# Kernel tuning notes

Hardware: AMD Instinct MI355X
Metric: run time of the kernel (lower is better)

## Reference

```python
import jax, jax.numpy as jnp
import numpy as np

H = 4  # num_heads
LN_EPS = 1e-5


def setup_inputs() -> dict:
    key = jax.random.key(0)
    ks = jax.random.split(key, 6)
    B, N, IN, OUT = 4, 2048, 256, 256
    return {
        "node_feats": jax.random.normal(ks[0], (B, N, IN), dtype=jnp.float32),
        "adj_matrix": jax.random.uniform(ks[1], (B, N, N), dtype=jnp.float32),
        "W_lin": jax.random.normal(ks[2], (IN, OUT), dtype=jnp.float32) * (IN ** -0.5),
        "b_lin": jnp.zeros((OUT,), dtype=jnp.float32),
        "W_q": jax.random.normal(ks[3], (IN, OUT), dtype=jnp.float32) * (IN ** -0.5),
        "W_k": jax.random.normal(ks[4], (IN, OUT), dtype=jnp.float32) * (IN ** -0.5),
        "ln_g": jnp.ones((OUT,), dtype=jnp.float32),
        "ln_b": jnp.zeros((OUT,), dtype=jnp.float32),
    }


def _heads(x, B, N):
    # [B,N,OUT] -> [B,H,N,hd]
    return x.reshape(B, N, H, -1).transpose(0, 2, 1, 3)


def reference(node_feats, adj_matrix, W_lin, b_lin, W_q, W_k, ln_g, ln_b):
    B, N, _ = node_feats.shape
    out_dim = W_lin.shape[1]
    hd = out_dim // H
    scale = hd ** -0.5
    lrelu = lambda z: jax.nn.leaky_relu(z, 0.01)

    X = _heads(lrelu(node_feats @ W_lin + b_lin), B, N)   # [B,H,N,hd]
    q = _heads(lrelu(node_feats @ W_q), B, N)
    k = _heads(lrelu(node_feats @ W_k), B, N)

    att = jax.nn.sigmoid(jnp.einsum('bhxd,bhyd->bhxy', q, k) * scale)
    adj_h = adj_matrix[:, None] * att                     # [B,H,N,N]

    # symmetric degree normalization: D^-1/2 A D^-1/2 (broadcast form of diag_embed matmuls)
    deg = jnp.sum(adj_h, axis=-1)                         # [B,H,N]
    dis = jnp.where(deg > 0, deg ** -0.5, 0.0)
    A = dis[..., :, None] * adj_h * dis[..., None, :]

    Y = jnp.einsum('bhxy,bhyd->bhxd', A, X)
    Y = Y.transpose(0, 2, 1, 3).reshape(B, N, out_dim)

    mu = jnp.mean(Y, axis=-1, keepdims=True)
    var = jnp.mean((Y - mu) ** 2, axis=-1, keepdims=True)
    return (Y - mu) * jax.lax.rsqrt(var + LN_EPS) * ln_g + ln_b
```

## Files before the change

kernel.cpp:

```cpp
#include <hip/hip_runtime.h>
#include <hip/hip_bf16.h>

#define B_   4
#define N_   2048
#define IN_  256
#define OUT_ 256
#define H_   4
#define HD_  64
#define LN_EPS 1e-5f

typedef __bf16 bf16x8 __attribute__((ext_vector_type(8)));
typedef float  f32x4  __attribute__((ext_vector_type(4)));
typedef unsigned short u16x8 __attribute__((ext_vector_type(8)));
typedef unsigned int   u32x4 __attribute__((ext_vector_type(4)));

__device__ __forceinline__ unsigned short f2bf(float x) {
    unsigned int u = __float_as_uint(x);
    return (unsigned short)((u + 0x7FFFu + ((u >> 16) & 1u)) >> 16);
}
__device__ __forceinline__ float bf2f(unsigned short u) {
    return __uint_as_float((unsigned int)u << 16);
}
__device__ __forceinline__ unsigned int cvtpk(float lo, float hi) {
    unsigned int r;
    asm("v_cvt_pk_bf16_f32 %0, %1, %2" : "=v"(r) : "v"(lo), "v"(hi));
    return r;
}

__global__ __launch_bounds__(256) void conv_kernel(
    const float* __restrict__ nf, const float* __restrict__ Wl,
    const float* __restrict__ Wq, const float* __restrict__ Wk,
    unsigned short* __restrict__ nfb, unsigned short* __restrict__ Wt)
{
    const int bid = blockIdx.x, tid = threadIdx.x;
    if (bid < 1024) {
        size_t i = ((size_t)bid * 256 + tid) * 8;
        u16x8 o;
        #pragma unroll
        for (int j = 0; j < 8; j++) o[j] = f2bf(nf[i + j]);
        *(u16x8*)&nfb[i] = o;
    } else {
        int t = (bid - 1024) * 256 + tid;
        int z = t >> 16;
        int l = t & 65535;
        int k = l & 255, n = l >> 8;
        const float* W = (z == 0) ? Wl : (z == 1 ? Wq : Wk);
        Wt[(size_t)z * 65536 + n * 256 + k] = f2bf(W[k * 256 + n]);
    }
}

__global__ __launch_bounds__(256) void gemm3_kernel(
    const unsigned short* __restrict__ nfb, const unsigned short* __restrict__ Wt3,
    const float* __restrict__ bl,
    unsigned short* __restrict__ qb, unsigned short* __restrict__ kb,
    unsigned short* __restrict__ Xt)
{
    const int z  = blockIdx.z;
    const int m0 = blockIdx.x * 64, n0 = blockIdx.y * 64;
    const int tid = threadIdx.x, wave = tid >> 6, lane = tid & 63;
    const int lq = lane >> 4, lr = lane & 15;
    const unsigned short* Wt = Wt3 + (size_t)z * 65536;

    f32x4 acc[4] = {};
    #pragma unroll 4
    for (int k0 = 0; k0 < IN_; k0 += 32) {
        bf16x8 af = *(const bf16x8*)&nfb[(size_t)(m0 + wave * 16 + lr) * IN_ + k0 + lq * 8];
        #pragma unroll
        for (int f = 0; f < 4; f++) {
            bf16x8 bfr = *(const bf16x8*)&Wt[(size_t)(n0 + f * 16 + lr) * IN_ + k0 + lq * 8];
            acc[f] = __builtin_amdgcn_mfma_f32_16x16x32_bf16(af, bfr, acc[f], 0, 0, 0);
        }
    }

    #pragma unroll
    for (int f = 0; f < 4; f++) {
        int c = n0 + f * 16 + lr;
        float bias = (z == 0) ? bl[c] : 0.0f;
        #pragma unroll
        for (int r = 0; r < 4; r++) {
            int m = m0 + wave * 16 + lq * 4 + r;
            float v = acc[f][r] + bias;
            v = (v >= 0.f) ? v : 0.01f * v;
            unsigned short bv = f2bf(v);
            if (z == 0) {
                int n = m & (N_ - 1);
                int h = c >> 6, d = c & 63;
                Xt[(((size_t)(m >> 11) * H_ + h) * HD_ + d) * N_ + n] = bv;
            } else {
                unsigned short* dst = (z == 1) ? qb : kb;
                dst[(size_t)m * OUT_ + c] = bv;
            }
        }
    }
}

__global__ __launch_bounds__(256) void att_kernel(
    const float* __restrict__ adj,
    const unsigned short* __restrict__ qb,
    const unsigned short* __restrict__ kb,
    unsigned short* __restrict__ W,
    float* __restrict__ degp,
    int b_base, int SH)
{
    const int s  = blockIdx.z;
    const int bg = b_base + (s >> 2);
    const int hg = s & 3;
    const int x0 = blockIdx.x * 128, y0 = blockIdx.y * 128;
    const int tid = threadIdx.x, wave = tid >> 6, lane = tid & 63;
    const int lq = lane >> 4, lr = lane & 15;
    const int wq = wave >> 1, wn = wave & 1;
    const int wx0 = x0 + wq * 64, wy0 = y0 + wn * 64;
    const float sc = -0.125f * 1.44269504088896f;

    const unsigned short* qrow = qb + (size_t)(bg * N_ + wx0) * OUT_ + hg * HD_;
    const unsigned short* krow = kb + (size_t)(bg * N_ + wy0) * OUT_ + hg * HD_;

    f32x4 acc[4][4] = {};
    #pragma unroll
    for (int ks = 0; ks < 2; ks++) {
        bf16x8 af[4], bf[4];
        #pragma unroll
        for (int mf = 0; mf < 4; mf++)
            af[mf] = *(const bf16x8*)&qrow[(size_t)(mf * 16 + lr) * OUT_ + ks * 32 + lq * 8];
        #pragma unroll
        for (int nf = 0; nf < 4; nf++)
            bf[nf] = *(const bf16x8*)&krow[(size_t)(nf * 16 + lr) * OUT_ + ks * 32 + lq * 8];
        #pragma unroll
        for (int mf = 0; mf < 4; mf++)
            #pragma unroll
            for (int nf = 0; nf < 4; nf++)
                acc[mf][nf] = __builtin_amdgcn_mfma_f32_16x16x32_bf16(af[mf], bf[nf], acc[mf][nf], 0, 0, 0);
    }

    unsigned short* Wp = W + (size_t)s * N_ * N_;
    #pragma unroll
    for (int mf = 0; mf < 4; mf++) {
        #pragma unroll
        for (int r = 0; r < 4; r++) {
            int x = wx0 + mf * 16 + lq * 4 + r;
            const float* arow = adj + ((size_t)bg * N_ + x) * N_ + wy0;
            unsigned short* wrow = Wp + (size_t)x * N_ + wy0;
            float sum = 0.f;
            #pragma unroll
            for (int nf = 0; nf < 4; nf++) {
                float a = arow[nf * 16 + lr];
                float att = __builtin_amdgcn_rcpf(1.f + exp2f(acc[mf][nf][r] * sc));
                float wv = a * att;
                sum += wv;
                wrow[nf * 16 + lr] = f2bf(wv);
            }
            sum += __shfl_xor(sum, 1); sum += __shfl_xor(sum, 2);
            sum += __shfl_xor(sum, 4); sum += __shfl_xor(sum, 8);
            if (lr == 0)
                degp[((size_t)(blockIdx.y * 2 + wn) * SH + s) * N_ + x] = sum;
        }
    }
}

__global__ __launch_bounds__(256) void degsum_kernel(
    const float* __restrict__ degp, float* __restrict__ dis, int b_base, int SH)
{
    int t = blockIdx.x * 256 + threadIdx.x;
    int s = t >> 11, x = t & (N_ - 1);
    float sum = 0.f;
    #pragma unroll
    for (int j = 0; j < 32; j++) sum += degp[((size_t)j * SH + s) * N_ + x];
    dis[((size_t)b_base * H_ + s) * N_ + x] = (sum > 0.f) ? rsqrtf(sum) : 0.f;
}

__global__ __launch_bounds__(256) void scale_kernel(
    const unsigned short* __restrict__ Xt, const float* __restrict__ dis,
    unsigned short* __restrict__ Xs)
{
    int t = blockIdx.x * 256 + threadIdx.x;
    size_t idx = (size_t)t * 8;
    int s = t >> 14;
    int y = (int)(idx & (N_ - 1));
    f32x4 d0 = *(const f32x4*)&dis[(size_t)s * N_ + y];
    f32x4 d1 = *(const f32x4*)&dis[(size_t)s * N_ + y + 4];
    u16x8 x = *(const u16x8*)&Xt[idx];
    u32x4 o;
    o[0] = cvtpk(bf2f(x[0]) * d0[0], bf2f(x[1]) * d0[1]);
    o[1] = cvtpk(bf2f(x[2]) * d0[2], bf2f(x[3]) * d0[3]);
    o[2] = cvtpk(bf2f(x[4]) * d1[0], bf2f(x[5]) * d1[1]);
    o[3] = cvtpk(bf2f(x[6]) * d1[2], bf2f(x[7]) * d1[3]);
    *(u32x4*)&Xs[idx] = o;
}

__global__ __launch_bounds__(512) void yout_kernel(
    const unsigned short* __restrict__ W,
    const unsigned short* __restrict__ Xs,
    const float* __restrict__ dis,
    float* __restrict__ Yraw,
    int b_base)
{
    const int s  = blockIdx.y;
    const int bg = b_base + (s >> 2);
    const int hg = s & 3;
    const int x0 = blockIdx.x * 32;
    const int tid = threadIdx.x;
    const int wave = tid >> 6, lane = tid & 63;
    const int xw = wave >> 2, dq = wave & 3;
    const int lq = lane >> 4, lr = lane & 15;

    __shared__ unsigned short As[2][32 * 256];

    const int srow = tid >> 4, kslot = tid & 15;
    const int swz  = (srow & 7) << 4;
    const unsigned short* Wrow =
        W + (size_t)s * N_ * N_ + (size_t)(x0 + srow) * N_ + kslot * 16;

    const unsigned short* Xp = Xs + ((size_t)s * HD_ + dq * 16 + lr) * N_;

    const int arow = xw * 16 + lr;
    const int arsw = (arow & 7) << 4;

    f32x4 Y = {};

    {
        u16x8 r0 = *(const u16x8*)&Wrow[0];
        u16x8 r1 = *(const u16x8*)&Wrow[8];
        char* base = (char*)&As[0][0] + srow * 512;
        *(u16x8*)(base + ((kslot * 32) ^ swz))      = r0;
        *(u16x8*)(base + ((kslot * 32 + 16) ^ swz)) = r1;
    }
    __syncthreads();

    int cur = 0;
    for (int kt = 0; kt < 8; kt++) {
        u16x8 n0, n1;
        if (kt < 7) {
            n0 = *(const u16x8*)&Wrow[(kt + 1) * 256];
            n1 = *(const u16x8*)&Wrow[(kt + 1) * 256 + 8];
        }
        const char* abase = (const char*)&As[cur][0] + arow * 512;
        #pragma unroll
        for (int half = 0; half < 2; half++) {
            bf16x8 xf[4];
            #pragma unroll
            for (int u = 0; u < 4; u++)
                xf[u] = *(const bf16x8*)&Xp[kt * 256 + (half * 4 + u) * 32 + lq * 8];
            #pragma unroll
            for (int u = 0; u < 4; u++) {
                const int kb = ((half * 4 + u) * 32 + lq * 8) * 2;
                bf16x8 af = *(const bf16x8*)(abase + (kb ^ arsw));
                Y = __builtin_amdgcn_mfma_f32_16x16x32_bf16(af, xf[u], Y, 0, 0, 0);
            }
        }
        if (kt < 7) {
            char* base = (char*)&As[cur ^ 1][0] + srow * 512;
            *(u16x8*)(base + ((kslot * 32) ^ swz))      = n0;
            *(u16x8*)(base + ((kslot * 32 + 16) ^ swz)) = n1;
        }
        __syncthreads();
        cur ^= 1;
    }

    #pragma unroll
    for (int r = 0; r < 4; r++) {
        int x = x0 + xw * 16 + lq * 4 + r;
        float dx = dis[((size_t)bg * H_ + hg) * N_ + x];
        Yraw[((size_t)(bg * N_ + x)) * OUT_ + hg * HD_ + dq * 16 + lr] = Y[r] * dx;
    }
}

__global__ __launch_bounds__(256) void ln_kernel(
    const float* __restrict__ Yraw,
    const float* __restrict__ lng, const float* __restrict__ lnb,
    float* __restrict__ out)
{
    const int row = blockIdx.x;
    const int c = threadIdx.x;
    const size_t base = (size_t)row * OUT_ + c;
    float v = Yraw[base];

    float s1 = v, s2 = v * v;
    #pragma unroll
    for (int d = 1; d < 64; d <<= 1) { s1 += __shfl_xor(s1, d); s2 += __shfl_xor(s2, d); }
    __shared__ float red[2][4];
    if ((c & 63) == 0) { red[0][c >> 6] = s1; red[1][c >> 6] = s2; }
    __syncthreads();
    float t1 = red[0][0] + red[0][1] + red[0][2] + red[0][3];
    float t2 = red[1][0] + red[1][1] + red[1][2] + red[1][3];
    float mu  = t1 * (1.f / 256.f);
    float var = t2 * (1.f / 256.f) - mu * mu;
    float rs  = rsqrtf(var + LN_EPS);
    out[base] = (v - mu) * rs * lng[c] + lnb[c];
}

extern "C" void kernel_launch(void* const* d_in, const int* in_sizes, int n_in,
                              void* d_out, int out_size, void* d_ws, size_t ws_size,
                              hipStream_t stream) {
    const float* nf  = (const float*)d_in[0];
    const float* adj = (const float*)d_in[1];
    const float* Wl  = (const float*)d_in[2];
    const float* bl  = (const float*)d_in[3];
    const float* Wq  = (const float*)d_in[4];
    const float* Wk  = (const float*)d_in[5];
    const float* lng = (const float*)d_in[6];
    const float* lnb = (const float*)d_in[7];
    float* out = (float*)d_out;

    char* w = (char*)d_ws;
    unsigned short* nfb = (unsigned short*)w;  w += (size_t)B_ * N_ * IN_ * 2;
    unsigned short* Wt  = (unsigned short*)w;  w += (size_t)3 * IN_ * OUT_ * 2;
    unsigned short* qb  = (unsigned short*)w;  w += (size_t)B_ * N_ * OUT_ * 2;
    unsigned short* kb  = (unsigned short*)w;  w += (size_t)B_ * N_ * OUT_ * 2;
    unsigned short* Xt  = (unsigned short*)w;  w += (size_t)B_ * N_ * OUT_ * 2;
    unsigned short* Xs  = (unsigned short*)w;  w += (size_t)B_ * N_ * OUT_ * 2;
    float* dis  = (float*)w;                   w += (size_t)B_ * H_ * N_ * 4;
    float* Yraw = (float*)w;                   w += (size_t)B_ * N_ * OUT_ * 4;
    size_t fixed = (size_t)(w - (char*)d_ws);

    size_t need4 = fixed + (size_t)32 * 16 * N_ * 4 + (size_t)16 * N_ * N_ * 2;
    int nb = (ws_size >= need4) ? 4 : 1;
    int SH = nb * H_;
    float* degp = (float*)w;                   w += (size_t)32 * SH * N_ * 4;
    unsigned short* Wbuf = (unsigned short*)w;

    conv_kernel <<<1792, 256, 0, stream>>>(nf, Wl, Wq, Wk, nfb, Wt);
    gemm3_kernel<<<dim3(128, 4, 3), 256, 0, stream>>>(nfb, Wt, bl, qb, kb, Xt);

    for (int b0 = 0; b0 < B_; b0 += nb) {
        size_t xoff = (size_t)b0 * H_ * HD_ * N_;
        att_kernel   <<<dim3(16, 16, SH), 256, 0, stream>>>(adj, qb, kb, Wbuf, degp, b0, SH);
        degsum_kernel<<<SH * N_ / 256, 256, 0, stream>>>(degp, dis, b0, SH);
        scale_kernel <<<SH * HD_ * N_ / 8 / 256, 256, 0, stream>>>(Xt + xoff, dis + (size_t)b0 * H_ * N_, Xs + xoff);
        yout_kernel  <<<dim3(N_ / 32, SH), 512, 0, stream>>>(Wbuf, Xs + xoff, dis, Yraw, b0);
    }
    ln_kernel<<<B_ * N_, 256, 0, stream>>>(Yraw, lng, lnb, out);
}
```

Baseline: 312.8 us.

## Stage adj tile in LDS, coalesce W stores, atomically accumulate degree

The attention kernel now loads the 128x128 adjacency tile into shared memory with coalesced float4 loads. It computes the sigmoid-weighted values in place in LDS and writes the bf16 W tile out as coalesced 16-byte rows, instead of scattered per-lane 2-byte loads and stores. The per-tile partial degree buffer and the degsum kernel are removed: row sums are accumulated with atomicAdd into a zeroed degree array, and rsqrt is taken lazily in the scale and output kernels. This removes one launch and the partial-sum traffic. In exchange it adds atomics, a memset, and rounds adj to bf16 before the multiply, which slightly changes precision.

Result: no change. 313.4 us (+0.2%).

```diff
diff --git a/kernel.cpp b/kernel.cpp
--- a/kernel.cpp
+++ b/kernel.cpp
@@ -12,6 +12,7 @@
 typedef __bf16 bf16x8 __attribute__((ext_vector_type(8)));
 typedef float  f32x4  __attribute__((ext_vector_type(4)));
 typedef unsigned short u16x8 __attribute__((ext_vector_type(8)));
+typedef unsigned int   u32x2 __attribute__((ext_vector_type(2)));
 typedef unsigned int   u32x4 __attribute__((ext_vector_type(4)));
 
 __device__ __forceinline__ unsigned short f2bf(float x) {
@@ -99,7 +100,7 @@
     const unsigned short* __restrict__ qb,
     const unsigned short* __restrict__ kb,
     unsigned short* __restrict__ W,
-    float* __restrict__ degp,
+    float* __restrict__ deg,
     int b_base, int SH)
 {
     const int s  = blockIdx.z;
@@ -109,88 +110,106 @@
     const int tid = threadIdx.x, wave = tid >> 6, lane = tid & 63;
     const int lq = lane >> 4, lr = lane & 15;
     const int wq = wave >> 1, wn = wave & 1;
-    const int wx0 = x0 + wq * 64, wy0 = y0 + wn * 64;
+    const int wx0 = wq * 64, wy0 = wn * 64;
     const float sc = -0.125f * 1.44269504088896f;
 
-    const unsigned short* qrow = qb + (size_t)(bg * N_ + wx0) * OUT_ + hg * HD_;
-    const unsigned short* krow = kb + (size_t)(bg * N_ + wy0) * OUT_ + hg * HD_;
-
+    __shared__ unsigned short ads[128][136];
+
+    {
+        const int row0 = tid >> 5;
+        const int col  = (tid & 31) * 4;
+        const float* ap = adj + ((size_t)bg * N_ + x0 + row0) * N_ + y0 + col;
+        #pragma unroll 4
+        for (int i = 0; i < 16; i++) {
+            f32x4 v = *(const f32x4*)(ap + (size_t)i * 8 * N_);
+            u32x2 p = { cvtpk(v[0], v[1]), cvtpk(v[2], v[3]) };
+            *(u32x2*)&ads[row0 + i * 8][col] = p;
+        }
+    }
+
+    const unsigned short* qrow = qb + (size_t)(bg * N_ + x0 + wx0) * OUT_ + hg * HD_;
+    const unsigned short* krow = kb + (size_t)(bg * N_ + y0 + wy0) * OUT_ + hg * HD_;
     f32x4 acc[4][4] = {};
     #pragma unroll
     for (int ks = 0; ks < 2; ks++) {
-        bf16x8 af[4], bf[4];
+        bf16x8 af[4];
         #pragma unroll
         for (int mf = 0; mf < 4; mf++)
             af[mf] = *(const bf16x8*)&qrow[(size_t)(mf * 16 + lr) * OUT_ + ks * 32 + lq * 8];
         #pragma unroll
-        for (int nf = 0; nf < 4; nf++)
-            bf[nf] = *(const bf16x8*)&krow[(size_t)(nf * 16 + lr) * OUT_ + ks * 32 + lq * 8];
-        #pragma unroll
-        for (int mf = 0; mf < 4; mf++)
+        for (int nf = 0; nf < 4; nf++) {
+            bf16x8 bfr = *(const bf16x8*)&krow[(size_t)(nf * 16 + lr) * OUT_ + ks * 32 + lq * 8];
             #pragma unroll
-            for (int nf = 0; nf < 4; nf++)
-                acc[mf][nf] = __builtin_amdgcn_mfma_f32_16x16x32_bf16(af[mf], bf[nf], acc[mf][nf], 0, 0, 0);
-    }
-
-    unsigned short* Wp = W + (size_t)s * N_ * N_;
+            for (int mf = 0; mf < 4; mf++)
+                acc[mf][nf] = __builtin_amdgcn_mfma_f32_16x16x32_bf16(af[mf], bfr, acc[mf][nf], 0, 0, 0);
+        }
+    }
+    __syncthreads();
+
+    float* degrow = deg + ((size_t)bg * H_ + hg) * N_ + x0;
     #pragma unroll
     for (int mf = 0; mf < 4; mf++) {
         #pragma unroll
         for (int r = 0; r < 4; r++) {
-            int x = wx0 + mf * 16 + lq * 4 + r;
-            const float* arow = adj + ((size_t)bg * N_ + x) * N_ + wy0;
-            unsigned short* wrow = Wp + (size_t)x * N_ + wy0;
+            const int xl = wx0 + mf * 16 + lq * 4 + r;
             float sum = 0.f;
             #pragma unroll
             for (int nf = 0; nf < 4; nf++) {
-                float a = arow[nf * 16 + lr];
+                const int yl = wy0 + nf * 16 + lr;
+                float a = bf2f(ads[xl][yl]);
                 float att = __builtin_amdgcn_rcpf(1.f + exp2f(acc[mf][nf][r] * sc));
                 float wv = a * att;
+                ads[xl][yl] = (unsigned short)cvtpk(wv, wv);
                 sum += wv;
-                wrow[nf * 16 + lr] = f2bf(wv);
             }
             sum += __shfl_xor(sum, 1); sum += __shfl_xor(sum, 2);
             sum += __shfl_xor(sum, 4); sum += __shfl_xor(sum, 8);
             if (lr == 0)
-                degp[((size_t)(blockIdx.y * 2 + wn) * SH + s) * N_ + x] = sum;
-        }
-    }
-}
-
-__global__ __launch_bounds__(256) void degsum_kernel(
-    const float* __restrict__ degp, float* __restrict__ dis, int b_base, int SH)
-{
-    int t = blockIdx.x * 256 + threadIdx.x;
-    int s = t >> 11, x = t & (N_ - 1);
-    float sum = 0.f;
-    #pragma unroll
-    for (int j = 0; j < 32; j++) sum += degp[((size_t)j * SH + s) * N_ + x];
-    dis[((size_t)b_base * H_ + s) * N_ + x] = (sum > 0.f) ? rsqrtf(sum) : 0.f;
+                atomicAdd(&degrow[xl], sum);
+        }
+    }
+    __syncthreads();
+
+    unsigned short* Wp = W + (size_t)s * N_ * N_;
+    const int col = (tid & 15) * 8;
+    const int r0  = tid >> 4;
+    #pragma unroll
+    for (int i = 0; i < 8; i++) {
+        int row = i * 16 + r0;
+        u16x8 v = *(const u16x8*)&ads[row][col];
+        *(u16x8*)&Wp[(size_t)(x0 + row) * N_ + y0 + col] = v;
+    }
 }
 
 __global__ __launch_bounds__(256) void scale_kernel(
-    const unsigned short* __restrict__ Xt, const float* __restrict__ dis,
+    const unsigned short* __restrict__ Xt, const float* __restrict__ deg,
     unsigned short* __restrict__ Xs)
 {
     int t = blockIdx.x * 256 + threadIdx.x;
     size_t idx = (size_t)t * 8;
     int s = t >> 14;
     int y = (int)(idx & (N_ - 1));
-    f32x4 d0 = *(const f32x4*)&dis[(size_t)s * N_ + y];
-    f32x4 d1 = *(const f32x4*)&dis[(size_t)s * N_ + y + 4];
+    f32x4 g0 = *(const f32x4*)&deg[(size_t)s * N_ + y];
+    f32x4 g1 = *(const f32x4*)&deg[(size_t)s * N_ + y + 4];
+    float dv[8];
+    #pragma unroll
+    for (int j = 0; j < 4; j++) {
+        dv[j]     = (g0[j] > 0.f) ? rsqrtf(g0[j]) : 0.f;
+        dv[4 + j] = (g1[j] > 0.f) ? rsqrtf(g1[j]) : 0.f;
+    }
     u16x8 x = *(const u16x8*)&Xt[idx];
     u32x4 o;
-    o[0] = cvtpk(bf2f(x[0]) * d0[0], bf2f(x[1]) * d0[1]);
-    o[1] = cvtpk(bf2f(x[2]) * d0[2], bf2f(x[3]) * d0[3]);
-    o[2] = cvtpk(bf2f(x[4]) * d1[0], bf2f(x[5]) * d1[1]);
-    o[3] = cvtpk(bf2f(x[6]) * d1[2], bf2f(x[7]) * d1[3]);
+    o[0] = cvtpk(bf2f(x[0]) * dv[0], bf2f(x[1]) * dv[1]);
+    o[1] = cvtpk(bf2f(x[2]) * dv[2], bf2f(x[3]) * dv[3]);
+    o[2] = cvtpk(bf2f(x[4]) * dv[4], bf2f(x[5]) * dv[5]);
+    o[3] = cvtpk(bf2f(x[6]) * dv[6], bf2f(x[7]) * dv[7]);
     *(u32x4*)&Xs[idx] = o;
 }
 
 __global__ __launch_bounds__(512) void yout_kernel(
     const unsigned short* __restrict__ W,
     const unsigned short* __restrict__ Xs,
-    const float* __restrict__ dis,
+    const float* __restrict__ deg,
     float* __restrict__ Yraw,
     int b_base)
 {
@@ -259,7 +278,8 @@
     #pragma unroll
     for (int r = 0; r < 4; r++) {
         int x = x0 + xw * 16 + lq * 4 + r;
-        float dx = dis[((size_t)bg * H_ + hg) * N_ + x];
+        float g = deg[((size_t)bg * H_ + hg) * N_ + x];
+        float dx = (g > 0.f) ? rsqrtf(g) : 0.f;
         Yraw[((size_t)(bg * N_ + x)) * OUT_ + hg * HD_ + dq * 16 + lr] = Y[r] * dx;
     }
 }
@@ -308,25 +328,24 @@
     unsigned short* kb  = (unsigned short*)w;  w += (size_t)B_ * N_ * OUT_ * 2;
     unsigned short* Xt  = (unsigned short*)w;  w += (size_t)B_ * N_ * OUT_ * 2;
     unsigned short* Xs  = (unsigned short*)w;  w += (size_t)B_ * N_ * OUT_ * 2;
-    float* dis  = (float*)w;                   w += (size_t)B_ * H_ * N_ * 4;
+    float* deg  = (float*)w;                   w += (size_t)B_ * H_ * N_ * 4;
     float* Yraw = (float*)w;                   w += (size_t)B_ * N_ * OUT_ * 4;
     size_t fixed = (size_t)(w - (char*)d_ws);
 
-    size_t need4 = fixed + (size_t)32 * 16 * N_ * 4 + (size_t)16 * N_ * N_ * 2;
+    size_t need4 = fixed + (size_t)16 * N_ * N_ * 2;
     int nb = (ws_size >= need4) ? 4 : 1;
     int SH = nb * H_;
-    float* degp = (float*)w;                   w += (size_t)32 * SH * N_ * 4;
     unsigned short* Wbuf = (unsigned short*)w;
 
+    hipMemsetAsync(deg, 0, (size_t)B_ * H_ * N_ * 4, stream);
     conv_kernel <<<1792, 256, 0, stream>>>(nf, Wl, Wq, Wk, nfb, Wt);
     gemm3_kernel<<<dim3(128, 4, 3), 256, 0, stream>>>(nfb, Wt, bl, qb, kb, Xt);
 
     for (int b0 = 0; b0 < B_; b0 += nb) {
         size_t xoff = (size_t)b0 * H_ * HD_ * N_;
-        att_kernel   <<<dim3(16, 16, SH), 256, 0, stream>>>(adj, qb, kb, Wbuf, degp, b0, SH);
-        degsum_kernel<<<SH * N_ / 256, 256, 0, stream>>>(degp, dis, b0, SH);
-        scale_kernel <<<SH * HD_ * N_ / 8 / 256, 256, 0, stream>>>(Xt + xoff, dis + (size_t)b0 * H_ * N_, Xs + xoff);
-        yout_kernel  <<<dim3(N_ / 32, SH), 512, 0, stream>>>(Wbuf, Xs + xoff, dis, Yraw, b0);
+        att_kernel  <<<dim3(16, 16, SH), 256, 0, stream>>>(adj, qb, kb, Wbuf, deg, b0, SH);
+        scale_kernel<<<SH * HD_ * N_ / 8 / 256, 256, 0, stream>>>(Xt + xoff, deg + (size_t)b0 * H_ * N_, Xs + xoff);
+        yout_kernel <<<dim3(N_ / 32, SH), 512, 0, stream>>>(Wbuf, Xs + xoff, deg, Yraw, b0);
     }
     ln_kernel<<<B_ * N_, 256, 0, stream>>>(Yraw, lng, lnb, out);
 }
```
